# Kernel optimization log

Measured on AMD Instinct MI355X. Metric: run time of the kernel, lower is better.

Reference implementation:

```python
import jax, jax.numpy as jnp
import numpy as np

KS = 3               # kernel_size
PAD = (KS - 1) // 2  # same padding
K2 = KS * KS
B, H, W = 4, 1024, 1024
SCALE = 1.0          # residual scale


def setup_inputs() -> dict:
    key = jax.random.key(0)
    k1, k2, k3 = jax.random.split(key, 3)
    init_dem = jax.random.normal(k1, (B, 1, H, W), jnp.float32)
    weight = jax.random.normal(k2, (B, K2, H, W), jnp.float32)          # modulation mask
    offset = jax.random.normal(k3, (B, 2 * K2, H, W), jnp.float32) * 2.0  # (dy,dx) per tap
    w = jnp.ones((1, 1, KS, KS), jnp.float32)   # nn.Parameter ones
    b = jnp.zeros((1,), jnp.float32)            # nn.Parameter zeros
    return {"init_dem": init_dem, "weight": weight, "offset": offset, "w": w, "b": b}


def _bilinear(img, y, x):
    # img: [H, W]; y, x: [H, W] fractional sample positions. Zero padding outside.
    Hh, Ww = img.shape
    y0 = jnp.floor(y)
    x0 = jnp.floor(x)

    def gather(yi, xi):
        valid = (yi >= 0) & (yi <= Hh - 1) & (xi >= 0) & (xi <= Ww - 1)
        yc = jnp.clip(yi, 0, Hh - 1).astype(jnp.int32)
        xc = jnp.clip(xi, 0, Ww - 1).astype(jnp.int32)
        return jnp.where(valid, img[yc, xc], 0.0)

    wy1 = y - y0
    wx1 = x - x0
    wy0 = 1.0 - wy1
    wx0 = 1.0 - wx1
    return (wy0 * wx0 * gather(y0, x0)
            + wy0 * wx1 * gather(y0, x0 + 1.0)
            + wy1 * wx0 * gather(y0 + 1.0, x0)
            + wy1 * wx1 * gather(y0 + 1.0, x0 + 1.0))


def reference(init_dem, weight, offset, w, b):
    # residual=True branch: zero-mean normalize the modulation mask over taps
    mask = weight - jnp.mean(weight, axis=1, keepdims=True)            # [B, K2, H, W]
    off = offset.reshape(B, K2, 2, H, W)                               # (dy, dx) per tap

    ky, kx = jnp.meshgrid(jnp.arange(KS), jnp.arange(KS), indexing="ij")
    ky = ky.reshape(-1).astype(jnp.float32)                            # [K2]
    kx = kx.reshape(-1).astype(jnp.float32)
    hh = jnp.arange(H, dtype=jnp.float32)[:, None]                     # [H, 1]
    ww = jnp.arange(W, dtype=jnp.float32)[None, :]                     # [1, W]

    # sample position for tap k at output pixel (h, w): p = p0 + k - pad + offset
    ys = (hh - PAD + ky[:, None, None])[None] + off[:, :, 0]           # [B, K2, H, W]
    xs = (ww - PAD + kx[:, None, None])[None] + off[:, :, 1]

    # vmap over batch (image varies) and taps (image shared)
    sample = jax.vmap(jax.vmap(_bilinear, in_axes=(None, 0, 0)),
                      in_axes=(0, 0, 0))(init_dem[:, 0], ys, xs)       # [B, K2, H, W]

    refined = jnp.einsum("bkhw,k->bhw", sample * mask, w.reshape(-1)) + b[0]
    return refined[:, None] + SCALE * init_dem                          # residual add
```

## Files before the change

kernel.cpp:

```cpp
#include <hip/hip_runtime.h>

#define BB 4
#define HH 1024
#define WW 1024
#define K2 9
#define PAD 1

#define R   12
#define TW  64
#define TH  4
#define RW  (TW + 2*R)
#define RH  (TH + 2*R)
#define RSZ (RW * RH)

__global__ __launch_bounds__(256, 4) void dcn_kernel(
    const float* __restrict__ init_dem,
    const float* __restrict__ weight,
    const float* __restrict__ offset,
    const float* __restrict__ wk,
    const float* __restrict__ bias,
    float* __restrict__ out)
{
    __shared__ float region[RSZ];

    const int HW = HH * WW;

    int i    = blockIdx.x;
    int b    = (i & 7) >> 1;
    int widx = ((i >> 3) << 1) | (i & 1);
    int tile_w = widx & 15;
    int tile_h = widx >> 4;
    int w0 = tile_w * TW;
    int h0 = tile_h * TH;

    const float* img = init_dem + (size_t)b * HW;

    const int tid = threadIdx.x;
    const int tx  = tid & 63;
    const int ty  = tid >> 6;
    const int h   = h0 + ty;
    const int w   = w0 + tx;
    const int rem = h * WW + w;

    const float* wq = weight + (size_t)b * K2 * HW + rem;
    const float* oq = offset + (size_t)b * 2 * K2 * HW + rem;

    float wt[K2], dy[K2], dx[K2];
#pragma unroll
    for (int k = 0; k < K2; ++k) {
        wt[k] = __builtin_nontemporal_load(wq + (size_t)k * HW);
        dy[k] = __builtin_nontemporal_load(oq + (size_t)(2 * k) * HW);
        dx[k] = __builtin_nontemporal_load(oq + (size_t)(2 * k + 1) * HW);
    }
    __builtin_amdgcn_sched_barrier(0);

#pragma unroll
    for (int it = 0; it < (RSZ + 255) / 256; ++it) {
        int e = tid + it * 256;
        if (e < RSZ) {
            int r = e / RW;
            int c = e - r * RW;
            int gy = h0 - R + r;
            int gx = w0 - R + c;
            float v = 0.f;
            if ((unsigned)gy < (unsigned)HH && (unsigned)gx < (unsigned)WW)
                v = img[gy * WW + gx];
            region[e] = v;
        }
    }
    __syncthreads();

    const float bval = bias[0];
    float wsum = 0.f;
#pragma unroll
    for (int k = 0; k < K2; ++k) wsum += wt[k];
    const float mean = wsum * (1.0f / K2);

    const float fy = (float)(ty + R - PAD);
    const float fx = (float)(tx + R - PAD);

    float acc = 0.f;
#pragma unroll
    for (int k = 0; k < K2; ++k) {
        const int ky = k / 3, kx = k % 3;

        float ysl = (fy + (float)ky) + dy[k];
        float xsl = (fx + (float)kx) + dx[k];

        float y0f = floorf(ysl);
        float x0f = floorf(xsl);
        float wy1 = ysl - y0f;
        float wx1 = xsl - x0f;
        float wy0 = 1.f - wy1;
        float wx0 = 1.f - wx1;

        int y0l = (int)y0f;
        int x0l = (int)x0f;

        float v00, v01, v10, v11;
        if (((unsigned)y0l < (unsigned)(RH - 1)) &
            ((unsigned)x0l < (unsigned)(RW - 1))) {
            int base = y0l * RW + x0l;
            v00 = region[base];
            v10 = region[base + RW];
            v01 = region[base + 1];
            v11 = region[base + RW + 1];
        } else {
            int y0g = y0l + (h0 - R);
            int x0g = x0l + (w0 - R);
            int y1g = y0g + 1;
            int x1g = x0g + 1;
            bool y0v = (y0g >= 0) & (y0g < HH);
            bool y1v = (y1g >= 0) & (y1g < HH);
            bool x0v = (x0g >= 0) & (x0g < WW);
            bool x1v = (x1g >= 0) & (x1g < WW);
            int yc0 = min(max(y0g, 0), HH - 1);
            int yc1 = min(max(y1g, 0), HH - 1);
            int xc0 = min(max(x0g, 0), WW - 1);
            int xc1 = min(max(x1g, 0), WW - 1);
            v00 = (y0v & x0v) ? img[(size_t)yc0 * WW + xc0] : 0.f;
            v01 = (y0v & x1v) ? img[(size_t)yc0 * WW + xc1] : 0.f;
            v10 = (y1v & x0v) ? img[(size_t)yc1 * WW + xc0] : 0.f;
            v11 = (y1v & x1v) ? img[(size_t)yc1 * WW + xc1] : 0.f;
        }

        float samp = wy0 * (wx0 * v00 + wx1 * v01)
                   + wy1 * (wx0 * v10 + wx1 * v11);
        acc += samp * (wt[k] - mean) * wk[k];
    }

    float resid = region[(ty + R) * RW + (tx + R)];
    float rres  = acc + bval + resid;
    __builtin_nontemporal_store(rres, out + (size_t)b * HW + rem);
}

extern "C" void kernel_launch(void* const* d_in, const int* in_sizes, int n_in,
                              void* d_out, int out_size, void* d_ws, size_t ws_size,
                              hipStream_t stream) {
    const float* init_dem = (const float*)d_in[0];
    const float* weight   = (const float*)d_in[1];
    const float* offset   = (const float*)d_in[2];
    const float* wk       = (const float*)d_in[3];
    const float* bias     = (const float*)d_in[4];
    float* out            = (float*)d_out;

    const int nblocks = BB * (WW / TW) * (HH / TH);
    dcn_kernel<<<dim3(nblocks), dim3(256), 0, stream>>>(init_dem, weight, offset, wk, bias, out);
}
```

Before: 108.8 us.

## Stage weight and offset channels into LDS via async global_load_lds

Instead of each thread doing 27 scalar nontemporal loads into registers, each wave issues 16-byte direct global-to-LDS loads of whole channel tiles into a new 27KB shared buffer, and threads read their values back from LDS after the sync. This is meant to cut VGPR pressure and use wider, asynchronous loads that overlap with the region staging. The larger LDS footprint (about 37KB per block) and the removal of the 4-blocks-per-CU launch bound may reduce occupancy.

```diff
diff --git a/kernel.cpp b/kernel.cpp
--- a/kernel.cpp
+++ b/kernel.cpp
@@ -13,7 +13,9 @@
 #define RH  (TH + 2*R)
 #define RSZ (RW * RH)
 
-__global__ __launch_bounds__(256, 4) void dcn_kernel(
+#define NCH 27
+
+__global__ __launch_bounds__(256) void dcn_kernel(
     const float* __restrict__ init_dem,
     const float* __restrict__ weight,
     const float* __restrict__ offset,
@@ -22,6 +24,7 @@
     float* __restrict__ out)
 {
     __shared__ float region[RSZ];
+    __shared__ float sbuf[NCH * 256];
 
     const int HW = HH * WW;
 
@@ -36,23 +39,26 @@
     const float* img = init_dem + (size_t)b * HW;
 
     const int tid = threadIdx.x;
-    const int tx  = tid & 63;
-    const int ty  = tid >> 6;
-    const int h   = h0 + ty;
-    const int w   = w0 + tx;
-    const int rem = h * WW + w;
+    const int wv  = tid >> 6;
+    const int ln  = tid & 63;
+    const int srow = ln >> 4;
+    const int scol = (ln & 15) << 2;
 
-    const float* wq = weight + (size_t)b * K2 * HW + rem;
-    const float* oq = offset + (size_t)b * 2 * K2 * HW + rem;
-
-    float wt[K2], dy[K2], dx[K2];
+    const float* wslab = weight + (size_t)b * K2 * HW     + (size_t)h0 * WW + w0;
+    const float* oslab = offset + (size_t)b * 2 * K2 * HW + (size_t)h0 * WW + w0;
 #pragma unroll
-    for (int k = 0; k < K2; ++k) {
-        wt[k] = __builtin_nontemporal_load(wq + (size_t)k * HW);
-        dy[k] = __builtin_nontemporal_load(oq + (size_t)(2 * k) * HW);
-        dx[k] = __builtin_nontemporal_load(oq + (size_t)(2 * k + 1) * HW);
+    for (int it = 0; it < 7; ++it) {
+        int c = wv + (it << 2);
+        if (c < NCH) {
+            const float* g = (c < 9) ? (wslab + (size_t)c * HW)
+                                     : (oslab + (size_t)(c - 9) * HW);
+            g += srow * WW + scol;
+            __builtin_amdgcn_global_load_lds(
+                (const __attribute__((address_space(1))) void*)g,
+                (__attribute__((address_space(3))) void*)&sbuf[c * 256],
+                16, 0, 0);
+        }
     }
-    __builtin_amdgcn_sched_barrier(0);
 
 #pragma unroll
     for (int it = 0; it < (RSZ + 255) / 256; ++it) {
@@ -70,22 +76,36 @@
     }
     __syncthreads();
 
-    const float bval = bias[0];
+    const int prow = tid >> 6;
+    const int pcol = tid & 63;
+    const int h    = h0 + prow;
+    const int w    = w0 + pcol;
+    const int rem  = h * WW + w;
+    const int sidx = prow * 64 + pcol;
+
+    float wt[K2];
     float wsum = 0.f;
 #pragma unroll
-    for (int k = 0; k < K2; ++k) wsum += wt[k];
+    for (int k = 0; k < K2; ++k) {
+        wt[k] = sbuf[k * 256 + sidx];
+        wsum += wt[k];
+    }
     const float mean = wsum * (1.0f / K2);
+    const float bval = bias[0];
 
-    const float fy = (float)(ty + R - PAD);
-    const float fx = (float)(tx + R - PAD);
+    const float fy = (float)(prow + R - PAD);
+    const float fx = (float)(pcol + R - PAD);
 
     float acc = 0.f;
 #pragma unroll
     for (int k = 0; k < K2; ++k) {
         const int ky = k / 3, kx = k % 3;
 
-        float ysl = (fy + (float)ky) + dy[k];
-        float xsl = (fx + (float)kx) + dx[k];
+        float dy = sbuf[(9 + 2 * k)  * 256 + sidx];
+        float dx = sbuf[(10 + 2 * k) * 256 + sidx];
+
+        float ysl = (fy + (float)ky) + dy;
+        float xsl = (fx + (float)kx) + dx;
 
         float y0f = floorf(ysl);
         float x0f = floorf(xsl);
@@ -129,7 +149,7 @@
         acc += samp * (wt[k] - mean) * wk[k];
     }
 
-    float resid = region[(ty + R) * RW + (tx + R)];
+    float resid = region[(prow + R) * RW + (pcol + R)];
     float rres  = acc + bval + resid;
     __builtin_nontemporal_store(rres, out + (size_t)b * HW + rem);
 }
```

Result: slower. 131.8 us (+21.2%).

## Process two rows per thread to amortize shared-memory halo tile loads

Applied to the files above, without the earlier changes.

Doubles the tile height so each thread computes two output pixels four rows apart. All 54 weight and offset values for both pixels are loaded up front to keep more memory requests in flight. The shared-memory image region, with its 12-pixel halo, now serves twice as many outputs, which cuts redundant halo loads per pixel. Launch bounds are raised to 5 blocks per CU and the tail guard on the region fill is dropped because the region size now divides evenly by 256. The cost is higher register pressure from the doubled per-thread inputs and half as many blocks.

```diff
diff --git a/kernel.cpp b/kernel.cpp
--- a/kernel.cpp
+++ b/kernel.cpp
@@ -8,12 +8,12 @@
 
 #define R   12
 #define TW  64
-#define TH  4
+#define TH  8
 #define RW  (TW + 2*R)
 #define RH  (TH + 2*R)
 #define RSZ (RW * RH)
 
-__global__ __launch_bounds__(256, 4) void dcn_kernel(
+__global__ __launch_bounds__(256, 5) void dcn_kernel(
     const float* __restrict__ init_dem,
     const float* __restrict__ weight,
     const float* __restrict__ offset,
@@ -38,100 +38,112 @@
     const int tid = threadIdx.x;
     const int tx  = tid & 63;
     const int ty  = tid >> 6;
-    const int h   = h0 + ty;
-    const int w   = w0 + tx;
-    const int rem = h * WW + w;
 
-    const float* wq = weight + (size_t)b * K2 * HW + rem;
-    const float* oq = offset + (size_t)b * 2 * K2 * HW + rem;
+    const int rem0 = (h0 + ty) * WW + w0 + tx;
+    const int rem1 = rem0 + 4 * WW;
 
-    float wt[K2], dy[K2], dx[K2];
+    const float* wq = weight + (size_t)b * K2 * HW;
+    const float* oq = offset + (size_t)b * 2 * K2 * HW;
+
+    float wt0[K2], dy0[K2], dx0[K2];
 #pragma unroll
     for (int k = 0; k < K2; ++k) {
-        wt[k] = __builtin_nontemporal_load(wq + (size_t)k * HW);
-        dy[k] = __builtin_nontemporal_load(oq + (size_t)(2 * k) * HW);
-        dx[k] = __builtin_nontemporal_load(oq + (size_t)(2 * k + 1) * HW);
+        wt0[k] = __builtin_nontemporal_load(wq + (size_t)k * HW + rem0);
+        dy0[k] = __builtin_nontemporal_load(oq + (size_t)(2 * k) * HW + rem0);
+        dx0[k] = __builtin_nontemporal_load(oq + (size_t)(2 * k + 1) * HW + rem0);
     }
-    __builtin_amdgcn_sched_barrier(0);
+    float wt1[K2], dy1[K2], dx1[K2];
+#pragma unroll
+    for (int k = 0; k < K2; ++k) {
+        wt1[k] = __builtin_nontemporal_load(wq + (size_t)k * HW + rem1);
+        dy1[k] = __builtin_nontemporal_load(oq + (size_t)(2 * k) * HW + rem1);
+        dx1[k] = __builtin_nontemporal_load(oq + (size_t)(2 * k + 1) * HW + rem1);
+    }
 
 #pragma unroll
-    for (int it = 0; it < (RSZ + 255) / 256; ++it) {
+    for (int it = 0; it < RSZ / 256; ++it) {
         int e = tid + it * 256;
-        if (e < RSZ) {
-            int r = e / RW;
-            int c = e - r * RW;
-            int gy = h0 - R + r;
-            int gx = w0 - R + c;
-            float v = 0.f;
-            if ((unsigned)gy < (unsigned)HH && (unsigned)gx < (unsigned)WW)
-                v = img[gy * WW + gx];
-            region[e] = v;
-        }
+        int r = e / RW;
+        int c = e - r * RW;
+        int gy = h0 - R + r;
+        int gx = w0 - R + c;
+        float v = 0.f;
+        if ((unsigned)gy < (unsigned)HH && (unsigned)gx < (unsigned)WW)
+            v = img[gy * WW + gx];
+        region[e] = v;
     }
     __syncthreads();
 
     const float bval = bias[0];
-    float wsum = 0.f;
-#pragma unroll
-    for (int k = 0; k < K2; ++k) wsum += wt[k];
-    const float mean = wsum * (1.0f / K2);
-
-    const float fy = (float)(ty + R - PAD);
     const float fx = (float)(tx + R - PAD);
 
-    float acc = 0.f;
 #pragma unroll
-    for (int k = 0; k < K2; ++k) {
-        const int ky = k / 3, kx = k % 3;
+    for (int p = 0; p < 2; ++p) {
+        const float* wt = p ? wt1 : wt0;
+        const float* dy = p ? dy1 : dy0;
+        const float* dx = p ? dx1 : dx0;
+        const int   rem = p ? rem1 : rem0;
+        const float fy  = (float)(ty + p * 4 + R - PAD);
 
-        float ysl = (fy + (float)ky) + dy[k];
-        float xsl = (fx + (float)kx) + dx[k];
+        float wsum = 0.f;
+#pragma unroll
+        for (int k = 0; k < K2; ++k) wsum += wt[k];
+        const float mean = wsum * (1.0f / K2);
 
-        float y0f = floorf(ysl);
-        float x0f = floorf(xsl);
-        float wy1 = ysl - y0f;
-        float wx1 = xsl - x0f;
-        float wy0 = 1.f - wy1;
-        float wx0 = 1.f - wx1;
+        float acc = 0.f;
+#pragma unroll
+        for (int k = 0; k < K2; ++k) {
+            const int ky = k / 3, kx = k % 3;
 
-        int y0l = (int)y0f;
-        int x0l = (int)x0f;
+            float ysl = (fy + (float)ky) + dy[k];
+            float xsl = (fx + (float)kx) + dx[k];
 
-        float v00, v01, v10, v11;
-        if (((unsigned)y0l < (unsigned)(RH - 1)) &
-            ((unsigned)x0l < (unsigned)(RW - 1))) {
-            int base = y0l * RW + x0l;
-            v00 = region[base];
-            v10 = region[base + RW];
-            v01 = region[base + 1];
-            v11 = region[base + RW + 1];
-        } else {
-            int y0g = y0l + (h0 - R);
-            int x0g = x0l + (w0 - R);
-            int y1g = y0g + 1;
-            int x1g = x0g + 1;
-            bool y0v = (y0g >= 0) & (y0g < HH);
-            bool y1v = (y1g >= 0) & (y1g < HH);
-            bool x0v = (x0g >= 0) & (x0g < WW);
-            bool x1v = (x1g >= 0) & (x1g < WW);
-            int yc0 = min(max(y0g, 0), HH - 1);
-            int yc1 = min(max(y1g, 0), HH - 1);
-            int xc0 = min(max(x0g, 0), WW - 1);
-            int xc1 = min(max(x1g, 0), WW - 1);
-            v00 = (y0v & x0v) ? img[(size_t)yc0 * WW + xc0] : 0.f;
-            v01 = (y0v & x1v) ? img[(size_t)yc0 * WW + xc1] : 0.f;
-            v10 = (y1v & x0v) ? img[(size_t)yc1 * WW + xc0] : 0.f;
-            v11 = (y1v & x1v) ? img[(size_t)yc1 * WW + xc1] : 0.f;
+            float y0f = floorf(ysl);
+            float x0f = floorf(xsl);
+            float wy1 = ysl - y0f;
+            float wx1 = xsl - x0f;
+            float wy0 = 1.f - wy1;
+            float wx0 = 1.f - wx1;
+
+            int y0l = (int)y0f;
+            int x0l = (int)x0f;
+
+            float v00, v01, v10, v11;
+            if (((unsigned)y0l < (unsigned)(RH - 1)) &
+                ((unsigned)x0l < (unsigned)(RW - 1))) {
+                int base = y0l * RW + x0l;
+                v00 = region[base];
+                v10 = region[base + RW];
+                v01 = region[base + 1];
+                v11 = region[base + RW + 1];
+            } else {
+                int y0g = y0l + (h0 - R);
+                int x0g = x0l + (w0 - R);
+                int y1g = y0g + 1;
+                int x1g = x0g + 1;
+                bool y0v = (y0g >= 0) & (y0g < HH);
+                bool y1v = (y1g >= 0) & (y1g < HH);
+                bool x0v = (x0g >= 0) & (x0g < WW);
+                bool x1v = (x1g >= 0) & (x1g < WW);
+                int yc0 = min(max(y0g, 0), HH - 1);
+                int yc1 = min(max(y1g, 0), HH - 1);
+                int xc0 = min(max(x0g, 0), WW - 1);
+                int xc1 = min(max(x1g, 0), WW - 1);
+                v00 = (y0v & x0v) ? img[(size_t)yc0 * WW + xc0] : 0.f;
+                v01 = (y0v & x1v) ? img[(size_t)yc0 * WW + xc1] : 0.f;
+                v10 = (y1v & x0v) ? img[(size_t)yc1 * WW + xc0] : 0.f;
+                v11 = (y1v & x1v) ? img[(size_t)yc1 * WW + xc1] : 0.f;
+            }
+
+            float samp = wy0 * (wx0 * v00 + wx1 * v01)
+                       + wy1 * (wx0 * v10 + wx1 * v11);
+            acc += samp * (wt[k] - mean) * wk[k];
         }
 
-        float samp = wy0 * (wx0 * v00 + wx1 * v01)
-                   + wy1 * (wx0 * v10 + wx1 * v11);
-        acc += samp * (wt[k] - mean) * wk[k];
+        float resid = region[(ty + p * 4 + R) * RW + (tx + R)];
+        float rres  = acc + bval + resid;
+        __builtin_nontemporal_store(rres, out + (size_t)b * HW + rem);
     }
-
-    float resid = region[(ty + R) * RW + (tx + R)];
-    float rres  = acc + bval + resid;
-    __builtin_nontemporal_store(rres, out + (size_t)b * HW + rem);
 }
 
 extern "C" void kernel_launch(void* const* d_in, const int* in_sizes, int n_in,
```

Result: slower. 228.6 us (+110.2%).
